# Performance work log

Measured on AMD Instinct MI355X. Metric: run time of the kernel, lower is better.

## Reference

```python
import jax, jax.numpy as jnp
import numpy as np

LOOP = 30  # kernel last-dim / loop count from original module

def setup_inputs() -> dict:
    key = jax.random.key(0)
    kB, k1, k2 = jax.random.split(key, 3)
    B = jax.random.normal(kB, (16, 64, 32, 32), dtype=jnp.float32)
    # torch.rand -> uniform [0,1)
    kernel1 = jax.random.uniform(k1, (64, 32, 32, LOOP), dtype=jnp.float32)
    kernel2 = jax.random.uniform(k2, (64, 32, 32, LOOP), dtype=jnp.float32)
    return {"B": B, "kernel1": kernel1, "kernel2": kernel2}

def reference(B, kernel1, kernel2):
    # fftshift over the 3 spatial dims, then the 30-iteration loop is batched:
    # move loop dim to front -> (30,64,32,32), broadcast against B (batch,64,32,32).
    Bs = jnp.fft.fftshift(B, axes=(-3, -2, -1))            # (batch,64,32,32)
    k1 = jnp.moveaxis(kernel1, -1, 0)                      # (30,64,32,32)
    k2 = jnp.moveaxis(kernel2, -1, 0)
    f1 = jnp.fft.fftn(Bs[:, None] * k1, axes=(-3, -2, -1))  # (batch,30,64,32,32) complex
    f2 = jnp.fft.fftn(Bs[:, None] * k2, axes=(-3, -2, -1))
    # complex multiply-accumulate over the loop dim
    return jnp.sum(f1 * f2, axis=1)                        # (batch,64,32,32) complex
```

## Files before the change

kernel.cpp:

```cpp
#include <hip/hip_runtime.h>
#include <hip/hip_fp16.h>
#include <cstdint>
#include <cstddef>


typedef unsigned int u32x4 __attribute__((ext_vector_type(4)));

__host__ __device__ constexpr float twc(int k) {
  switch (k & 31) {
    case 0: return 1.0f;        case 1: return 0.98078528f;
    case 2: return 0.92387953f; case 3: return 0.83146961f;
    case 4: return 0.70710678f; case 5: return 0.55557023f;
    case 6: return 0.38268343f; case 7: return 0.19509032f;
    case 8: return 0.0f;        case 9: return -0.19509032f;
    case 10: return -0.38268343f; case 11: return -0.55557023f;
    case 12: return -0.70710678f; case 13: return -0.83146961f;
    case 14: return -0.92387953f; case 15: return -0.98078528f;
    default: return 0.0f;
  }
}
__host__ __device__ constexpr float tws(int k) {
  switch (k & 31) {
    case 0: return 0.0f;        case 1: return 0.19509032f;
    case 2: return 0.38268343f; case 3: return 0.55557023f;
    case 4: return 0.70710678f; case 5: return 0.83146961f;
    case 6: return 0.92387953f; case 7: return 0.98078528f;
    case 8: return 1.0f;        case 9: return 0.98078528f;
    case 10: return 0.92387953f; case 11: return 0.83146961f;
    case 12: return 0.70710678f; case 13: return 0.55557023f;
    case 14: return 0.38268343f; case 15: return 0.19509032f;
    default: return 0.0f;
  }
}

constexpr int brN(int x, int bits) {
  int r = 0;
  for (int b = 0; b < bits; ++b) { r = (r << 1) | (x & 1); x >>= 1; }
  return r;
}

template <int N>
__device__ __forceinline__ void fftN(float* xr, float* xi) {
#pragma unroll
  for (int len = 2; len <= N; len <<= 1) {
    const int half = len >> 1;
    const int step = 32 / len;
#pragma unroll
    for (int g = 0; g < N; g += len) {
#pragma unroll
      for (int j = 0; j < half; ++j) {
        const float c = twc(j * step), s = tws(j * step);
        const int lo = g + j, hi = g + j + half;
        float vr = xr[hi] * c + xi[hi] * s;
        float vi = xi[hi] * c - xr[hi] * s;
        float ur = xr[lo], ui = xi[lo];
        xr[lo] = ur + vr; xi[lo] = ui + vi;
        xr[hi] = ur - vr; xi[hi] = ui - vi;
      }
    }
  }
}

__device__ __forceinline__ unsigned h2u(__half2 h) {
  union { __half2 h; unsigned u; } c; c.h = h; return c.u;
}
__device__ __forceinline__ float2 u2f2(unsigned u) {
  union { unsigned u; __half2 h; } c; c.u = u; return __half22float2(c.h);
}

__global__ __launch_bounds__(256) void kzero(float4* __restrict__ o, int n4) {
  int i = blockIdx.x * 256 + threadIdx.x;
  if (i < n4) o[i] = make_float4(0.f, 0.f, 0.f, 0.f);
}


__global__ __launch_bounds__(256) void kpack(const float* __restrict__ k1,
                                             const float* __restrict__ k2,
                                             unsigned* __restrict__ kch) {
  int d0 = blockIdx.x >> 5, d1 = blockIdx.x & 31;
  __shared__ unsigned s[960];
  int base = (d0 * 32 + d1) * 960;
  for (int u = threadIdx.x; u < 960; u += 256)
    s[u] = h2u(__float22half2_rn(make_float2(k1[base + u], k2[base + u])));
  __syncthreads();
  for (int w = threadIdx.x; w < 960; w += 256) {
    int i = w >> 5, d2 = w & 31;
    kch[((size_t)(i * 64 + d0) * 32 + d1) * 32 + d2] = s[d2 * 30 + i];
  }
}

__global__ __launch_bounds__(128, 4) void kfft2d_ws(
    const float* __restrict__ B, const unsigned* __restrict__ kch,
    __half2* __restrict__ Z, int j0) {
  __shared__ __half2 Ms[4][32 * 33];

  const int t = threadIdx.x;
  const int v = blockIdx.x >> 4;
  const int q2 = blockIdx.x & 15;
  const int job = j0 + v;
  const int b = job / 30;
  const int i = job - b * 30;

  const int s = t >> 5;
  const int lc = t & 31;
  const int n0 = (q2 << 2) | s;

  const float* Bb = B + ((size_t)b << 16);

  float xr[32], xi[32];

  {
    const int sn0 = (n0 + 32) & 63;
    const float* bp = Bb + (sn0 << 10);
    const int sc = (lc + 16) & 31;
    const unsigned* kcl = kch + (((size_t)i << 6 | n0) << 10);

    float breg[32];
    unsigned kreg[32];
#pragma unroll
    for (int n1 = 0; n1 < 32; ++n1) {
      breg[n1] = bp[(((n1 + 16) & 31) << 5) | sc];
      kreg[n1] = kcl[(n1 << 5) | lc];
    }
#pragma unroll
    for (int n1 = 0; n1 < 32; ++n1) {
      float2 kv = u2f2(kreg[n1]);
      xr[brN(n1, 5)] = breg[n1] * kv.x;
      xi[brN(n1, 5)] = breg[n1] * kv.y;
    }
    fftN<32>(xr, xi);
#pragma unroll
    for (int u = 0; u < 32; ++u)
      Ms[s][u * 33 + lc] = __float22half2_rn(make_float2(xr[u], xi[u]));
  }
  __syncthreads();

  {
    const int r = lc;
#pragma unroll
    for (int j = 0; j < 32; ++j) {
      float2 q = __half22float2(Ms[s][r * 33 + j]);
      xr[brN(j, 5)] = q.x;
      xi[brN(j, 5)] = q.y;
    }
    fftN<32>(xr, xi);

    __half2* zrow = Z + (((size_t)v << 16) | (n0 << 10) | (r << 5));
    u32x4* z4 = reinterpret_cast<u32x4*>(zrow);
#pragma unroll
    for (int k = 0; k < 8; ++k) {
      __half2 h0 = __float22half2_rn(make_float2(xr[4 * k + 0], xi[4 * k + 0]));
      __half2 h1 = __float22half2_rn(make_float2(xr[4 * k + 1], xi[4 * k + 1]));
      __half2 h2 = __float22half2_rn(make_float2(xr[4 * k + 2], xi[4 * k + 2]));
      __half2 h3 = __float22half2_rn(make_float2(xr[4 * k + 3], xi[4 * k + 3]));
      u32x4 pk = {h2u(h0), h2u(h1), h2u(h2), h2u(h3)};
      z4[k] = pk;
    }
  }
}

__global__ __launch_bounds__(256) void kacc64(const __half2* __restrict__ Z,
                                              float* __restrict__ tmp,
                                              int b0, int cb) {
  __shared__ float Ar[64 * 33], Ai[64 * 33];
  __shared__ float Br[64 * 33], Bi[64 * 33];
  __shared__ float W64c[64], W64s[64];

  const int t = threadIdx.x;
  const int d1 = blockIdx.x & 31;
  const int r = blockIdx.x >> 5;
  const int bl = r % cb;
  const int ig = r / cb;
  const int b = b0 + bl;
  const int i0g = ig * 8;
  const int i1g = (i0g + 8) < 30 ? (i0g + 8) : 30;

  if (t < 64) {
    float sv, cv;
    __sincosf(6.283185307179586f / 64.0f * (float)t, &sv, &cv);
    W64c[t] = cv; W64s[t] = sv;
  }
  __syncthreads();

  const int qc = t >> 5;
  const int d2 = t & 31;

  float acc[8];
#pragma unroll
  for (int a = 0; a < 8; ++a) acc[a] = 0.f;

  for (int i = i0g; i < i1g; ++i) {
    const int v = bl * 30 + i;
    const __half2* zv = Z + (((size_t)v << 16) | (d1 << 5));
#pragma unroll
    for (int j = 0; j < 8; ++j) {
      int f = (j << 8) | t;
      int rd0 = f >> 5, rc = f & 31;
      float2 w = __half22float2(zv[((size_t)rd0 << 10) | rc]);
      Ar[rd0 * 33 + rc] = w.x;
      Ai[rd0 * 33 + rc] = w.y;
    }
    __syncthreads();

    {
      float xr[8], xi[8];
#pragma unroll
      for (int u = 0; u < 8; ++u) {
        int n0 = qc + (brN(u, 3) << 3);
        xr[u] = Ar[n0 * 33 + d2]; xi[u] = Ai[n0 * 33 + d2];
      }
      fftN<8>(xr, xi);
#pragma unroll
      for (int c = 0; c < 8; ++c) {
        int m = (qc * c) & 63;
        float wc = W64c[m], ws = W64s[m];
        float hr = xr[c] * wc + xi[c] * ws;
        float hi = xi[c] * wc - xr[c] * ws;
        int q2 = (c << 3) | qc;
        Br[q2 * 33 + d2] = hr; Bi[q2 * 33 + d2] = hi;
      }
    }
    __syncthreads();

    {
      float xr[8], xi[8];
#pragma unroll
      for (int u = 0; u < 8; ++u) {
        int q2 = (qc << 3) | brN(u, 3);
        xr[u] = Br[q2 * 33 + d2]; xi[u] = Bi[q2 * 33 + d2];
      }
      fftN<8>(xr, xi);
#pragma unroll
      for (int a = 0; a < 8; ++a)
        acc[a] += 2.0f * xr[a] * xi[a];
    }
    __syncthreads();
  }

#pragma unroll
  for (int a = 0; a < 8; ++a) {
    int d0f = qc + (a << 3);
    size_t off = ((size_t)(b << 6 | d0f) << 10) | (d1 << 5) | d2;
    atomicAdd(&tmp[off], 0.25f * acc[a]);
  }
}

__global__ __launch_bounds__(256) void ksym(const float* __restrict__ tmp,
                                            float* __restrict__ out,
                                            int out_size) {
  int idx = blockIdx.x * 256 + threadIdx.x;
  if (idx >= out_size || idx >= 16 * 65536) return;
  int d2 = idx & 31, d1 = (idx >> 5) & 31, d0 = (idx >> 10) & 63, b = idx >> 16;
  int n = (b << 16) | (((64 - d0) & 63) << 10) | (((32 - d1) & 31) << 5) |
          ((32 - d2) & 31);
  out[idx] = tmp[idx] + tmp[n];
}

__global__ __launch_bounds__(256) void kfused(const float* __restrict__ B,
                                              const float* __restrict__ k1,
                                              const float* __restrict__ k2,
                                              float* __restrict__ out,
                                              int out_size) {
  __shared__ float Lr[4][32 * 33];
  __shared__ float Li[4][32 * 33];
  __shared__ float W64c[64], W64s[64];

  const int t = threadIdx.x;
  const int bid = blockIdx.x;
  const int b = bid & 15;
  const int iq = (bid >> 4) & 3;
  const int ns = bid >> 6;
  const int i0 = iq * 8;
  const int ni = (iq == 3) ? 6 : 8;
  const int k0base = ns * 8;

  if (t < 64) {
    float sv, cv;
    __sincosf(6.283185307179586f / 64.0f * (float)t, &sv, &cv);
    W64c[t] = cv; W64s[t] = sv;
  }
  __syncthreads();

  const int g = t >> 6;
  const int bc = t & 31;
  const int hh = (t >> 5) & 1;
  const int fs = t >> 5;
  const int fr = t & 31;
  const int w1 = t >> 5;
  const int w2 = t & 31;

  const float* Bb = B + ((size_t)b << 16);

  float Sig[8][4];
#pragma unroll
  for (int kg = 0; kg < 8; ++kg)
#pragma unroll
    for (int q = 0; q < 4; ++q) Sig[kg][q] = 0.f;

  for (int ii = 0; ii < ni; ++ii) {
    const int i = i0 + ii;

    float Zr[8][4], Zi[8][4];
#pragma unroll
    for (int kg = 0; kg < 8; ++kg)
#pragma unroll
      for (int q = 0; q < 4; ++q) { Zr[kg][q] = 0.f; Zi[kg][q] = 0.f; }

    for (int it = 0; it < 16; ++it) {
      const int n0 = (it << 2) | g;
      {
        const int sn0 = (n0 + 32) & 63;
        const float* bp = Bb + (sn0 << 10);
        const int sc = (bc + 16) & 31;
#pragma unroll
        for (int v = 0; v < 16; ++v) {
          const int n1 = (hh << 4) | v;
          float bv = bp[(((n1 + 16) & 31) << 5) | sc];
          int ke = (((n0 << 10) | (n1 << 5) | bc) * 30) + i;
          Lr[g][n1 * 33 + bc] = bv * k1[ke];
          Li[g][n1 * 33 + bc] = bv * k2[ke];
        }
      }
      __syncthreads();

      if (t < 128) {
        float xr[32], xi[32];
#pragma unroll
        for (int u = 0; u < 32; ++u) {
          int p = fr * 33 + brN(u, 5);
          xr[u] = Lr[fs][p]; xi[u] = Li[fs][p];
        }
        fftN<32>(xr, xi);
#pragma unroll
        for (int u = 0; u < 32; ++u) {
          int p = fr * 33 + u;
          Lr[fs][p] = xr[u]; Li[fs][p] = xi[u];
        }
      }
      __syncthreads();

      if (t < 128) {
        float xr[32], xi[32];
#pragma unroll
        for (int u = 0; u < 32; ++u) {
          int p = brN(u, 5) * 33 + fr;
          xr[u] = Lr[fs][p]; xi[u] = Li[fs][p];
        }
        fftN<32>(xr, xi);
#pragma unroll
        for (int u = 0; u < 32; ++u) {
          int p = u * 33 + fr;
          Lr[fs][p] = xr[u]; Li[fs][p] = xi[u];
        }
      }
      __syncthreads();

#pragma unroll 1
      for (int sq = 0; sq < 4; ++sq) {
        const int n0s = (it << 2) | sq;
        const int dm = n0s & 63;
        float yr[4], yi[4];
#pragma unroll
        for (int q = 0; q < 4; ++q) {
          int p = (w1 + (q << 3)) * 33 + w2;
          yr[q] = Lr[sq][p]; yi[q] = Li[sq][p];
        }
        int m = (k0base * n0s) & 63;
#pragma unroll
        for (int kg = 0; kg < 8; ++kg) {
          float c = W64c[m], sn = W64s[m];
#pragma unroll
          for (int q = 0; q < 4; ++q) {
            Zr[kg][q] += yr[q] * c + yi[q] * sn;
            Zi[kg][q] += yi[q] * c - yr[q] * sn;
          }
          m = (m + dm) & 63;
        }
      }
      __syncthreads();
    }

#pragma unroll
    for (int kg = 0; kg < 8; ++kg)
#pragma unroll
      for (int q = 0; q < 4; ++q)
        Sig[kg][q] += 2.0f * Zr[kg][q] * Zi[kg][q];
  }

#pragma unroll
  for (int kg = 0; kg < 8; ++kg) {
    const int k0 = k0base + kg;
    const int nk0 = (64 - k0) & 63;
#pragma unroll
    for (int q = 0; q < 4; ++q) {
      const int r1 = w1 + (q << 3);
      const float v = Sig[kg][q] * 0.25f;
      const int nr1 = (32 - r1) & 31;
      const int nw2 = (32 - w2) & 31;
      int off = (((b << 6) | k0) << 10) | (r1 << 5) | w2;
      int noff = (((b << 6) | nk0) << 10) | (nr1 << 5) | nw2;
      if (off < out_size) atomicAdd(&out[off], v);
      if (noff < out_size) atomicAdd(&out[noff], v);
    }
  }
}

extern "C" void kernel_launch(void* const* d_in, const int* in_sizes, int n_in,
                              void* d_out, int out_size, void* d_ws,
                              size_t ws_size, hipStream_t stream) {
  const float* B = (const float*)d_in[0];
  const float* k1 = (const float*)d_in[1];
  const float* k2 = (const float*)d_in[2];
  (void)in_sizes; (void)n_in;

  const size_t tmpB = 4ull << 20;
  const size_t Z1 = 30ull * 65536 * 4;
  const size_t kcB = 30ull * 65536 * 4;

  int nbcap = 0;
  if (ws_size >= tmpB + kcB + Z1)
    nbcap = (int)((ws_size - tmpB - kcB) / Z1);

  if (nbcap >= 1) {
    char* ws = (char*)d_ws;
    float* tmp = (float*)ws;
    unsigned* kch = (unsigned*)(ws + tmpB);
    __half2* Z = (__half2*)(ws + tmpB + kcB);
    int nb = nbcap > 16 ? 16 : nbcap;

    kzero<<<(out_size / 4 + 255) / 256, 256, 0, stream>>>((float4*)tmp,
                                                          out_size / 4);
    kpack<<<2048, 256, 0, stream>>>(k1, k2, kch);

    for (int b0 = 0; b0 < 16; b0 += nb) {
      int cb = (16 - b0) < nb ? (16 - b0) : nb;
      int j0 = b0 * 30;
      kfft2d_ws<<<cb * 30 * 16, 128, 0, stream>>>(B, kch, Z, j0);
      kacc64<<<cb * 32 * 4, 256, 0, stream>>>(Z, tmp, b0, cb);
    }

    ksym<<<(out_size + 255) / 256, 256, 0, stream>>>(tmp, (float*)d_out,
                                                     out_size);
  } else {
    int n4 = out_size >> 2;
    int zb = (n4 + 255) >> 8;
    if (zb > 0) kzero<<<zb, 256, 0, stream>>>((float4*)d_out, n4);
    kfused<<<512, 256, 0, stream>>>(B, k1, k2, (float*)d_out, out_size);
  }
}
```

Baseline: 106.2 us.

## Loop six loop-indices per FFT block, reusing B loads and prefetching kernel slices

Each kfft2d_ws block now handles six consecutive loop indices for one batch and channel-quad, instead of one. The B column is loaded once and reused across all six, and the next kernel slice is prefetched into registers while the current FFT runs. This cuts redundant B reads and block launch overhead, but the grid shrinks sixfold (cb*80 blocks), which reduces parallelism. Dropping the occupancy hint in launch_bounds, together with the extra live registers, may also lower occupancy.

Measured after the change: 108.0 us. About the same (+1.6%).

```diff
diff --git a/kernel.cpp b/kernel.cpp
--- a/kernel.cpp
+++ b/kernel.cpp
@@ -89,73 +89,89 @@
   }
 }
 
-__global__ __launch_bounds__(128, 4) void kfft2d_ws(
+__global__ __launch_bounds__(128) void kfft2d_ws(
     const float* __restrict__ B, const unsigned* __restrict__ kch,
-    __half2* __restrict__ Z, int j0) {
+    __half2* __restrict__ Z, int b0) {
   __shared__ __half2 Ms[4][32 * 33];
 
   const int t = threadIdx.x;
-  const int v = blockIdx.x >> 4;
   const int q2 = blockIdx.x & 15;
-  const int job = j0 + v;
-  const int b = job / 30;
-  const int i = job - b * 30;
+  const int r = blockIdx.x >> 4;
+  const int ig = r % 5;
+  const int bl = r / 5;
+  const int b = b0 + bl;
 
   const int s = t >> 5;
   const int lc = t & 31;
   const int n0 = (q2 << 2) | s;
 
-  const float* Bb = B + ((size_t)b << 16);
-
-  float xr[32], xi[32];
-
+  float breg[32];
   {
     const int sn0 = (n0 + 32) & 63;
-    const float* bp = Bb + (sn0 << 10);
+    const float* bp = B + ((size_t)b << 16) + (sn0 << 10);
     const int sc = (lc + 16) & 31;
-    const unsigned* kcl = kch + (((size_t)i << 6 | n0) << 10);
-
-    float breg[32];
-    unsigned kreg[32];
-#pragma unroll
-    for (int n1 = 0; n1 < 32; ++n1) {
+#pragma unroll
+    for (int n1 = 0; n1 < 32; ++n1)
       breg[n1] = bp[(((n1 + 16) & 31) << 5) | sc];
-      kreg[n1] = kcl[(n1 << 5) | lc];
-    }
+  }
+
+  const unsigned* kc0 = kch + (((size_t)(ig * 6) << 6 | n0) << 10);
+  unsigned kreg[32];
+#pragma unroll
+  for (int n1 = 0; n1 < 32; ++n1)
+    kreg[n1] = kc0[(n1 << 5) | lc];
+
+  for (int ii = 0; ii < 6; ++ii) {
+    float xr[32], xi[32];
+
 #pragma unroll
     for (int n1 = 0; n1 < 32; ++n1) {
       float2 kv = u2f2(kreg[n1]);
       xr[brN(n1, 5)] = breg[n1] * kv.x;
       xi[brN(n1, 5)] = breg[n1] * kv.y;
     }
+
+    if (ii < 5) {
+      const unsigned* kn = kc0 + ((size_t)(ii + 1) << 16);
+#pragma unroll
+      for (int n1 = 0; n1 < 32; ++n1)
+        kreg[n1] = kn[(n1 << 5) | lc];
+    }
+
     fftN<32>(xr, xi);
 #pragma unroll
     for (int u = 0; u < 32; ++u)
       Ms[s][u * 33 + lc] = __float22half2_rn(make_float2(xr[u], xi[u]));
-  }
-  __syncthreads();
-
-  {
-    const int r = lc;
-#pragma unroll
-    for (int j = 0; j < 32; ++j) {
-      float2 q = __half22float2(Ms[s][r * 33 + j]);
-      xr[brN(j, 5)] = q.x;
-      xi[brN(j, 5)] = q.y;
-    }
-    fftN<32>(xr, xi);
-
-    __half2* zrow = Z + (((size_t)v << 16) | (n0 << 10) | (r << 5));
-    u32x4* z4 = reinterpret_cast<u32x4*>(zrow);
-#pragma unroll
-    for (int k = 0; k < 8; ++k) {
-      __half2 h0 = __float22half2_rn(make_float2(xr[4 * k + 0], xi[4 * k + 0]));
-      __half2 h1 = __float22half2_rn(make_float2(xr[4 * k + 1], xi[4 * k + 1]));
-      __half2 h2 = __float22half2_rn(make_float2(xr[4 * k + 2], xi[4 * k + 2]));
-      __half2 h3 = __float22half2_rn(make_float2(xr[4 * k + 3], xi[4 * k + 3]));
-      u32x4 pk = {h2u(h0), h2u(h1), h2u(h2), h2u(h3)};
-      z4[k] = pk;
-    }
+    __syncthreads();
+
+    {
+      const int rr = lc;
+#pragma unroll
+      for (int j = 0; j < 32; ++j) {
+        float2 q = __half22float2(Ms[s][rr * 33 + j]);
+        xr[brN(j, 5)] = q.x;
+        xi[brN(j, 5)] = q.y;
+      }
+      fftN<32>(xr, xi);
+
+      const int v = bl * 30 + ig * 6 + ii;
+      __half2* zrow = Z + (((size_t)v << 16) | (n0 << 10) | (rr << 5));
+      u32x4* z4 = reinterpret_cast<u32x4*>(zrow);
+#pragma unroll
+      for (int k = 0; k < 8; ++k) {
+        __half2 h0 =
+            __float22half2_rn(make_float2(xr[4 * k + 0], xi[4 * k + 0]));
+        __half2 h1 =
+            __float22half2_rn(make_float2(xr[4 * k + 1], xi[4 * k + 1]));
+        __half2 h2 =
+            __float22half2_rn(make_float2(xr[4 * k + 2], xi[4 * k + 2]));
+        __half2 h3 =
+            __float22half2_rn(make_float2(xr[4 * k + 3], xi[4 * k + 3]));
+        u32x4 pk = {h2u(h0), h2u(h1), h2u(h2), h2u(h3)};
+        z4[k] = pk;
+      }
+    }
+    __syncthreads();
   }
 }
 
@@ -434,8 +450,7 @@
 
     for (int b0 = 0; b0 < 16; b0 += nb) {
       int cb = (16 - b0) < nb ? (16 - b0) : nb;
-      int j0 = b0 * 30;
-      kfft2d_ws<<<cb * 30 * 16, 128, 0, stream>>>(B, kch, Z, j0);
+      kfft2d_ws<<<cb * 80, 128, 0, stream>>>(B, kch, Z, b0);
       kacc64<<<cb * 32 * 4, 256, 0, stream>>>(Z, tmp, b0, cb);
     }
 
```
